# Performance work log

Hardware: AMD Instinct MI355X
Metric: run time of the kernel (lower is better)

The kernel has to match this reference:

```python
import jax, jax.numpy as jnp
import numpy as np

B, S, HLEN, VLEN, HID = 32, 2048, 1024, 1024, 1024


def setup_inputs() -> dict:
    key = jax.random.key(0)
    ks = jax.random.split(key, 6)
    scale_W = 1.0 / np.sqrt(HLEN)
    scale_U = 1.0 / np.sqrt(VLEN)
    scale_w = 1.0 / np.sqrt(HID)
    return {
        "h": jax.random.normal(ks[0], (B, HLEN), dtype=jnp.float32),
        "V": jax.random.normal(ks[1], (B, S, VLEN), dtype=jnp.float32),
        "W_w": jax.random.normal(ks[2], (HID, HLEN), dtype=jnp.float32) * scale_W,
        "W_b": jax.random.normal(ks[3], (HID,), dtype=jnp.float32) * scale_W,
        "U_w": jax.random.normal(ks[4], (HID, VLEN), dtype=jnp.float32) * scale_U,
        "w_w": jax.random.normal(ks[5], (HID,), dtype=jnp.float32) * scale_w,
    }


def reference(h, V, W_w, W_b, U_w, w_w):
    # e = w^T tanh(W h + U V^T + b); beta = softmax(e); out = sum_s beta_s V_s
    h_proj = h @ W_w.T + W_b                      # [B, HID]
    V_proj = jnp.einsum('bsv,dv->bsd', V, U_w)    # [B, S, HID]
    e = jnp.einsum('bsd,d->bs', jnp.tanh(h_proj[:, None, :] + V_proj), w_w)  # [B, S]
    beta = jax.nn.softmax(e, axis=1)              # [B, S]
    return jnp.einsum('bs,bsv->bv', beta, V)      # [B, VLEN]
```

## Files before the change

### kernel.cpp

```cpp
#include <hip/hip_runtime.h>

constexpr int B_   = 32;
constexpr int S_   = 2048;
constexpr int HID_ = 1024;
constexpr int VL_  = 1024;

typedef __attribute__((ext_vector_type(4))) float  f32x4;
typedef __attribute__((ext_vector_type(4))) short  s16x4;
typedef __attribute__((ext_vector_type(8))) short  s16x8;

__device__ __forceinline__ short f2bf(float f) {
    union { float f; unsigned u; } v; v.f = f;
    unsigned r = v.u + 0x7fffu + ((v.u >> 16) & 1u);
    return (short)(r >> 16);
}

__device__ __forceinline__ float fast_tanh(float x) {
    float e2 = __expf(2.0f * x);
    return 1.0f - 2.0f / (e2 + 1.0f);
}

__device__ __forceinline__ void async_cp16(const void* g, void* l) {
    __builtin_amdgcn_global_load_lds(
        (const __attribute__((address_space(1))) unsigned int*)g,
        (__attribute__((address_space(3))) unsigned int*)l,
        16, 0, 0);
}

__global__ __launch_bounds__(256) void hproj_kernel(const float* __restrict__ h,
                                                    const float* __restrict__ Ww,
                                                    const float* __restrict__ Wb,
                                                    float* __restrict__ hp) {
    int tid = threadIdx.x;
    int wave = tid >> 6, lane = tid & 63;
    int d = blockIdx.x * 4 + wave;
    const float* wr = Ww + (size_t)d * HID_;
    float4 wreg[4];
#pragma unroll
    for (int i = 0; i < 4; i++) wreg[i] = *(const float4*)(wr + i * 256 + lane * 4);
    float bias = Wb[d];
    for (int b = 0; b < B_; b++) {
        const float* hr = h + (size_t)b * HID_;
        float acc = 0.0f;
#pragma unroll
        for (int i = 0; i < 4; i++) {
            float4 x = *(const float4*)(hr + i * 256 + lane * 4);
            acc += wreg[i].x * x.x + wreg[i].y * x.y + wreg[i].z * x.z + wreg[i].w * x.w;
        }
#pragma unroll
        for (int o = 32; o; o >>= 1) acc += __shfl_xor(acc, o);
        if (lane == 0) hp[(size_t)b * HID_ + d] = acc + bias;
    }
}

__global__ __launch_bounds__(256) void cvt_kernel(const float* __restrict__ src,
                                                  short* __restrict__ dst, size_t n4) {
    size_t i = (size_t)blockIdx.x * blockDim.x + threadIdx.x;
    size_t stride = (size_t)gridDim.x * blockDim.x;
    for (; i < n4; i += stride) {
        float4 x = ((const float4*)src)[i];
        s16x4 y;
        y.x = f2bf(x.x); y.y = f2bf(x.y); y.z = f2bf(x.z); y.w = f2bf(x.w);
        ((s16x4*)dst)[i] = y;
    }
}

__global__ __launch_bounds__(256) void e_kernel_bf16(const short* __restrict__ Vm,
                                                     const short* __restrict__ Um,
                                                     const float* __restrict__ hp,
                                                     const float* __restrict__ ww,
                                                     float* __restrict__ e) {
    __shared__ short As[128][32];
    __shared__ short Bs[128][32];

    int tid = threadIdx.x;
    int b  = blockIdx.z;
    int d0 = blockIdx.x * 128;
    int s0 = blockIdx.y * 128;
    int wave = tid >> 6, lane = tid & 63;
    int wm = wave >> 1, wn = wave & 1;
    int col = lane & 15, quad = lane >> 4;

    f32x4 zero = {0.f, 0.f, 0.f, 0.f};
    f32x4 acc[4][4];
#pragma unroll
    for (int i = 0; i < 4; i++)
#pragma unroll
        for (int j = 0; j < 4; j++) acc[i][j] = zero;

    int r0 = 32 * wave + (lane >> 2);
    int kc = (lane & 3) * 8;
    const short* gA0 = Vm + ((size_t)b * S_ + s0 + r0) * VL_ + kc;
    const short* gA1 = gA0 + 16 * (size_t)VL_;
    const short* gB0 = Um + ((size_t)d0 + r0) * VL_ + kc;
    const short* gB1 = gB0 + 16 * (size_t)VL_;
    short* lA0 = &As[32 * wave][0];
    short* lA1 = &As[32 * wave + 16][0];
    short* lB0 = &Bs[32 * wave][0];
    short* lB1 = &Bs[32 * wave + 16][0];

    for (int k0 = 0; k0 < VL_; k0 += 32) {
        async_cp16(gA0, lA0);
        async_cp16(gA1, lA1);
        async_cp16(gB0, lB0);
        async_cp16(gB1, lB1);
        gA0 += 32; gA1 += 32; gB0 += 32; gB1 += 32;
        __syncthreads();

        s16x8 a8[4], b8[4];
#pragma unroll
        for (int tm = 0; tm < 4; tm++)
            a8[tm] = *(const s16x8*)&As[wm * 64 + tm * 16 + col][quad * 8];
#pragma unroll
        for (int tn = 0; tn < 4; tn++)
            b8[tn] = *(const s16x8*)&Bs[wn * 64 + tn * 16 + col][quad * 8];
#pragma unroll
        for (int tm = 0; tm < 4; tm++)
#pragma unroll
            for (int tn = 0; tn < 4; tn++)
                acc[tm][tn] = __builtin_amdgcn_mfma_f32_16x16x32_bf16(
                    a8[tm], b8[tn], acc[tm][tn], 0, 0, 0);
        __syncthreads();
    }

    float wv[4], hv[4];
#pragma unroll
    for (int tn = 0; tn < 4; tn++) {
        int d = d0 + wn * 64 + tn * 16 + col;
        wv[tn] = ww[d];
        hv[tn] = hp[(size_t)b * HID_ + d];
    }
#pragma unroll
    for (int tm = 0; tm < 4; tm++) {
#pragma unroll
        for (int reg = 0; reg < 4; reg++) {
            float p = 0.0f;
#pragma unroll
            for (int tn = 0; tn < 4; tn++)
                p += wv[tn] * fast_tanh(hv[tn] + acc[tm][tn][reg]);
            p += __shfl_xor(p, 1);
            p += __shfl_xor(p, 2);
            p += __shfl_xor(p, 4);
            p += __shfl_xor(p, 8);
            if (col == 0) {
                int s = s0 + wm * 64 + tm * 16 + quad * 4 + reg;
                atomicAdd(&e[(size_t)b * S_ + s], p);
            }
        }
    }
}

__global__ __launch_bounds__(256) void e_kernel_f32(const float* __restrict__ Vm,
                                                    const float* __restrict__ Um,
                                                    const float* __restrict__ hp,
                                                    const float* __restrict__ ww,
                                                    float* __restrict__ e) {
    __shared__ short As[128][40];
    __shared__ short Bs[128][40];
    int tid = threadIdx.x;
    int b  = blockIdx.z;
    int d0 = blockIdx.x * 128;
    int s0 = blockIdx.y * 128;
    int wave = tid >> 6, lane = tid & 63;
    int wm = wave >> 1, wn = wave & 1;
    int col = lane & 15, quad = lane >> 4;

    f32x4 zero = {0.f, 0.f, 0.f, 0.f};
    f32x4 acc[4][4];
#pragma unroll
    for (int i = 0; i < 4; i++)
#pragma unroll
        for (int j = 0; j < 4; j++) acc[i][j] = zero;

    const float* Abase = Vm + ((size_t)b * S_ + s0) * (size_t)VL_;
    const float* Bbase = Um + (size_t)d0 * (size_t)VL_;

    for (int k0 = 0; k0 < VL_; k0 += 32) {
        int k4 = tid & 7, rb = tid >> 3;
#pragma unroll
        for (int i = 0; i < 4; i++) {
            int r = rb + 32 * i;
            float4 x = *(const float4*)(Abase + (size_t)r * VL_ + k0 + k4 * 4);
            s16x4 ya; ya.x = f2bf(x.x); ya.y = f2bf(x.y); ya.z = f2bf(x.z); ya.w = f2bf(x.w);
            *(s16x4*)&As[r][k4 * 4] = ya;
            float4 y = *(const float4*)(Bbase + (size_t)r * VL_ + k0 + k4 * 4);
            s16x4 yb; yb.x = f2bf(y.x); yb.y = f2bf(y.y); yb.z = f2bf(y.z); yb.w = f2bf(y.w);
            *(s16x4*)&Bs[r][k4 * 4] = yb;
        }
        __syncthreads();
        s16x8 a8[4], b8[4];
#pragma unroll
        for (int tm = 0; tm < 4; tm++)
            a8[tm] = *(const s16x8*)&As[wm * 64 + tm * 16 + col][quad * 8];
#pragma unroll
        for (int tn = 0; tn < 4; tn++)
            b8[tn] = *(const s16x8*)&Bs[wn * 64 + tn * 16 + col][quad * 8];
#pragma unroll
        for (int tm = 0; tm < 4; tm++)
#pragma unroll
            for (int tn = 0; tn < 4; tn++)
                acc[tm][tn] = __builtin_amdgcn_mfma_f32_16x16x32_bf16(
                    a8[tm], b8[tn], acc[tm][tn], 0, 0, 0);
        __syncthreads();
    }

    float wv[4], hv[4];
#pragma unroll
    for (int tn = 0; tn < 4; tn++) {
        int d = d0 + wn * 64 + tn * 16 + col;
        wv[tn] = ww[d];
        hv[tn] = hp[(size_t)b * HID_ + d];
    }
#pragma unroll
    for (int tm = 0; tm < 4; tm++) {
#pragma unroll
        for (int reg = 0; reg < 4; reg++) {
            float p = 0.0f;
#pragma unroll
            for (int tn = 0; tn < 4; tn++)
                p += wv[tn] * fast_tanh(hv[tn] + acc[tm][tn][reg]);
            p += __shfl_xor(p, 1);
            p += __shfl_xor(p, 2);
            p += __shfl_xor(p, 4);
            p += __shfl_xor(p, 8);
            if (col == 0) {
                int s = s0 + wm * 64 + tm * 16 + quad * 4 + reg;
                atomicAdd(&e[(size_t)b * S_ + s], p);
            }
        }
    }
}

__global__ __launch_bounds__(256) void softmax_kernel(float* __restrict__ e) {
    int b = blockIdx.x, tid = threadIdx.x;
    float* row = e + (size_t)b * S_;
    float v[8];
    float m = -1e30f;
#pragma unroll
    for (int i = 0; i < 8; i++) { v[i] = row[tid + i * 256]; m = fmaxf(m, v[i]); }
#pragma unroll
    for (int o = 32; o; o >>= 1) m = fmaxf(m, __shfl_xor(m, o));
    __shared__ float rm[4], rs[4];
    int wave = tid >> 6, lane = tid & 63;
    if (lane == 0) rm[wave] = m;
    __syncthreads();
    m = fmaxf(fmaxf(rm[0], rm[1]), fmaxf(rm[2], rm[3]));
    float s = 0.0f;
#pragma unroll
    for (int i = 0; i < 8; i++) { v[i] = __expf(v[i] - m); s += v[i]; }
#pragma unroll
    for (int o = 32; o; o >>= 1) s += __shfl_xor(s, o);
    if (lane == 0) rs[wave] = s;
    __syncthreads();
    s = rs[0] + rs[1] + rs[2] + rs[3];
    float inv = 1.0f / s;
#pragma unroll
    for (int i = 0; i < 8; i++) row[tid + i * 256] = v[i] * inv;
}

__global__ __launch_bounds__(256) void out_kernel(const float* __restrict__ beta,
                                                  const float* __restrict__ V,
                                                  float* __restrict__ out) {
    int b = blockIdx.x, sc = blockIdx.y;
    int v4 = threadIdx.x;
    const float* Vb = V + ((size_t)b * S_ + (size_t)sc * 128) * VL_;
    const float* bb = beta + (size_t)b * S_ + (size_t)sc * 128;
    float ax = 0.f, ay = 0.f, az = 0.f, aw = 0.f;
    for (int s = 0; s < 128; s++) {
        float w = bb[s];
        float4 x = *(const float4*)(Vb + (size_t)s * VL_ + v4 * 4);
        ax += w * x.x; ay += w * x.y; az += w * x.z; aw += w * x.w;
    }
    float* o = out + (size_t)b * VL_ + v4 * 4;
    atomicAdd(o + 0, ax);
    atomicAdd(o + 1, ay);
    atomicAdd(o + 2, az);
    atomicAdd(o + 3, aw);
}

extern "C" void kernel_launch(void* const* d_in, const int* in_sizes, int n_in,
                              void* d_out, int out_size, void* d_ws, size_t ws_size,
                              hipStream_t stream) {
    const float* h  = (const float*)d_in[0];
    const float* V  = (const float*)d_in[1];
    const float* Ww = (const float*)d_in[2];
    const float* Wb = (const float*)d_in[3];
    const float* Uw = (const float*)d_in[4];
    const float* ww = (const float*)d_in[5];
    float* out = (float*)d_out;

    char* ws = (char*)d_ws;
    float* hp = (float*)ws;
    float* e  = (float*)(ws + 131072);
    short* Vb16 = (short*)(ws + 393216);
    short* Ub16 = Vb16 + (size_t)B_ * S_ * VL_;
    size_t need = 393216 + ((size_t)B_ * S_ * VL_ + (size_t)HID_ * VL_) * 2;
    bool bf16path = (ws_size >= need);

    hipMemsetAsync(e, 0, (size_t)B_ * S_ * 4, stream);
    hipMemsetAsync(out, 0, (size_t)out_size * 4, stream);

    hproj_kernel<<<dim3(HID_ / 4), 256, 0, stream>>>(h, Ww, Wb, hp);

    if (bf16path) {
        cvt_kernel<<<2048, 256, 0, stream>>>(V, Vb16, (size_t)B_ * S_ * VL_ / 4);
        cvt_kernel<<<256, 256, 0, stream>>>(Uw, Ub16, (size_t)HID_ * VL_ / 4);
        e_kernel_bf16<<<dim3(HID_ / 128, S_ / 128, B_), 256, 0, stream>>>(
            Vb16, Ub16, hp, ww, e);
    } else {
        e_kernel_f32<<<dim3(HID_ / 128, S_ / 128, B_), 256, 0, stream>>>(
            V, Uw, hp, ww, e);
    }

    softmax_kernel<<<B_, 256, 0, stream>>>(e);
    out_kernel<<<dim3(B_, S_ / 128), 256, 0, stream>>>(e, V, out);
}
```

Before: 667.6 us.

## Loop HID tiles inside e kernel and read bf16 V in output pass

```diff
diff --git a/kernel.cpp b/kernel.cpp
--- a/kernel.cpp
+++ b/kernel.cpp
@@ -13,6 +13,12 @@
     union { float f; unsigned u; } v; v.f = f;
     unsigned r = v.u + 0x7fffu + ((v.u >> 16) & 1u);
     return (short)(r >> 16);
+}
+
+__device__ __forceinline__ float bf2f(short s) {
+    union { unsigned u; float f; } v;
+    v.u = ((unsigned)(unsigned short)s) << 16;
+    return v.f;
 }
 
 __device__ __forceinline__ float fast_tanh(float x) {
@@ -72,82 +78,99 @@
                                                      float* __restrict__ e) {
     __shared__ short As[128][32];
     __shared__ short Bs[128][32];
+    __shared__ float ebuf[2][128];
 
     int tid = threadIdx.x;
-    int b  = blockIdx.z;
-    int d0 = blockIdx.x * 128;
-    int s0 = blockIdx.y * 128;
+    int s0 = blockIdx.x * 128;
+    int b  = blockIdx.y;
     int wave = tid >> 6, lane = tid & 63;
     int wm = wave >> 1, wn = wave & 1;
     int col = lane & 15, quad = lane >> 4;
 
-    f32x4 zero = {0.f, 0.f, 0.f, 0.f};
-    f32x4 acc[4][4];
-#pragma unroll
-    for (int i = 0; i < 4; i++)
-#pragma unroll
-        for (int j = 0; j < 4; j++) acc[i][j] = zero;
-
     int r0 = 32 * wave + (lane >> 2);
     int kc = (lane & 3) * 8;
-    const short* gA0 = Vm + ((size_t)b * S_ + s0 + r0) * VL_ + kc;
-    const short* gA1 = gA0 + 16 * (size_t)VL_;
-    const short* gB0 = Um + ((size_t)d0 + r0) * VL_ + kc;
-    const short* gB1 = gB0 + 16 * (size_t)VL_;
+    const short* gAb = Vm + ((size_t)b * S_ + s0 + r0) * VL_ + kc;
     short* lA0 = &As[32 * wave][0];
     short* lA1 = &As[32 * wave + 16][0];
     short* lB0 = &Bs[32 * wave][0];
     short* lB1 = &Bs[32 * wave + 16][0];
 
-    for (int k0 = 0; k0 < VL_; k0 += 32) {
-        async_cp16(gA0, lA0);
-        async_cp16(gA1, lA1);
-        async_cp16(gB0, lB0);
-        async_cp16(gB1, lB1);
-        gA0 += 32; gA1 += 32; gB0 += 32; gB1 += 32;
-        __syncthreads();
-
-        s16x8 a8[4], b8[4];
+    float ep[4][4];
+#pragma unroll
+    for (int i = 0; i < 4; i++)
+#pragma unroll
+        for (int j = 0; j < 4; j++) ep[i][j] = 0.0f;
+
+    for (int dt = 0; dt < 8; dt++) {
+        int d0 = dt * 128;
+        const short* gA0 = gAb;
+        const short* gA1 = gAb + 16 * (size_t)VL_;
+        const short* gB0 = Um + ((size_t)d0 + r0) * VL_ + kc;
+        const short* gB1 = gB0 + 16 * (size_t)VL_;
+
+        f32x4 zero = {0.f, 0.f, 0.f, 0.f};
+        f32x4 acc[4][4];
+#pragma unroll
+        for (int i = 0; i < 4; i++)
+#pragma unroll
+            for (int j = 0; j < 4; j++) acc[i][j] = zero;
+
+        for (int k0 = 0; k0 < VL_; k0 += 32) {
+            async_cp16(gA0, lA0);
+            async_cp16(gA1, lA1);
+            async_cp16(gB0, lB0);
+            async_cp16(gB1, lB1);
+            gA0 += 32; gA1 += 32; gB0 += 32; gB1 += 32;
+            __syncthreads();
+
+            s16x8 a8[4], b8[4];
+#pragma unroll
+            for (int tm = 0; tm < 4; tm++)
+                a8[tm] = *(const s16x8*)&As[wm * 64 + tm * 16 + col][quad * 8];
+#pragma unroll
+            for (int tn = 0; tn < 4; tn++)
+                b8[tn] = *(const s16x8*)&Bs[wn * 64 + tn * 16 + col][quad * 8];
+#pragma unroll
+            for (int tm = 0; tm < 4; tm++)
+#pragma unroll
+                for (int tn = 0; tn < 4; tn++)
+                    acc[tm][tn] = __builtin_amdgcn_mfma_f32_16x16x32_bf16(
+                        a8[tm], b8[tn], acc[tm][tn], 0, 0, 0);
+            __syncthreads();
+        }
+
+        float wv[4], hv[4];
+#pragma unroll
+        for (int tn = 0; tn < 4; tn++) {
+            int d = d0 + wn * 64 + tn * 16 + col;
+            wv[tn] = ww[d];
+            hv[tn] = hp[(size_t)b * HID_ + d];
+        }
 #pragma unroll
         for (int tm = 0; tm < 4; tm++)
-            a8[tm] = *(const s16x8*)&As[wm * 64 + tm * 16 + col][quad * 8];
-#pragma unroll
-        for (int tn = 0; tn < 4; tn++)
-            b8[tn] = *(const s16x8*)&Bs[wn * 64 + tn * 16 + col][quad * 8];
-#pragma unroll
-        for (int tm = 0; tm < 4; tm++)
-#pragma unroll
-            for (int tn = 0; tn < 4; tn++)
-                acc[tm][tn] = __builtin_amdgcn_mfma_f32_16x16x32_bf16(
-                    a8[tm], b8[tn], acc[tm][tn], 0, 0, 0);
-        __syncthreads();
-    }
-
-    float wv[4], hv[4];
-#pragma unroll
-    for (int tn = 0; tn < 4; tn++) {
-        int d = d0 + wn * 64 + tn * 16 + col;
-        wv[tn] = ww[d];
-        hv[tn] = hp[(size_t)b * HID_ + d];
-    }
-#pragma unroll
-    for (int tm = 0; tm < 4; tm++) {
+#pragma unroll
+            for (int reg = 0; reg < 4; reg++) {
+#pragma unroll
+                for (int tn = 0; tn < 4; tn++)
+                    ep[tm][reg] += wv[tn] * fast_tanh(hv[tn] + acc[tm][tn][reg]);
+            }
+    }
+
+#pragma unroll
+    for (int tm = 0; tm < 4; tm++)
 #pragma unroll
         for (int reg = 0; reg < 4; reg++) {
-            float p = 0.0f;
-#pragma unroll
-            for (int tn = 0; tn < 4; tn++)
-                p += wv[tn] * fast_tanh(hv[tn] + acc[tm][tn][reg]);
+            float p = ep[tm][reg];
             p += __shfl_xor(p, 1);
             p += __shfl_xor(p, 2);
             p += __shfl_xor(p, 4);
             p += __shfl_xor(p, 8);
-            if (col == 0) {
-                int s = s0 + wm * 64 + tm * 16 + quad * 4 + reg;
-                atomicAdd(&e[(size_t)b * S_ + s], p);
-            }
-        }
-    }
+            if (col == 0)
+                ebuf[wn][wm * 64 + tm * 16 + quad * 4 + reg] = p;
+        }
+    __syncthreads();
+    if (tid < 128)
+        e[(size_t)b * S_ + s0 + tid] = ebuf[0][tid] + ebuf[1][tid];
 }
 
 __global__ __launch_bounds__(256) void e_kernel_f32(const float* __restrict__ Vm,
@@ -258,9 +281,30 @@
     for (int i = 0; i < 8; i++) row[tid + i * 256] = v[i] * inv;
 }
 
-__global__ __launch_bounds__(256) void out_kernel(const float* __restrict__ beta,
-                                                  const float* __restrict__ V,
-                                                  float* __restrict__ out) {
+__global__ __launch_bounds__(256) void out_kernel_bf16(const float* __restrict__ beta,
+                                                       const short* __restrict__ Vb16,
+                                                       float* __restrict__ out) {
+    int b = blockIdx.x, sc = blockIdx.y;
+    int v4 = threadIdx.x;
+    const short* Vp = Vb16 + ((size_t)b * S_ + (size_t)sc * 128) * VL_;
+    const float* bb = beta + (size_t)b * S_ + (size_t)sc * 128;
+    float ax = 0.f, ay = 0.f, az = 0.f, aw = 0.f;
+    for (int s = 0; s < 128; s++) {
+        float w = bb[s];
+        s16x4 x = *(const s16x4*)(Vp + (size_t)s * VL_ + v4 * 4);
+        ax += w * bf2f(x.x); ay += w * bf2f(x.y);
+        az += w * bf2f(x.z); aw += w * bf2f(x.w);
+    }
+    float* o = out + (size_t)b * VL_ + v4 * 4;
+    atomicAdd(o + 0, ax);
+    atomicAdd(o + 1, ay);
+    atomicAdd(o + 2, az);
+    atomicAdd(o + 3, aw);
+}
+
+__global__ __launch_bounds__(256) void out_kernel_f32(const float* __restrict__ beta,
+                                                      const float* __restrict__ V,
+                                                      float* __restrict__ out) {
     int b = blockIdx.x, sc = blockIdx.y;
     int v4 = threadIdx.x;
     const float* Vb = V + ((size_t)b * S_ + (size_t)sc * 128) * VL_;
@@ -297,7 +341,6 @@
     size_t need = 393216 + ((size_t)B_ * S_ * VL_ + (size_t)HID_ * VL_) * 2;
     bool bf16path = (ws_size >= need);
 
-    hipMemsetAsync(e, 0, (size_t)B_ * S_ * 4, stream);
     hipMemsetAsync(out, 0, (size_t)out_size * 4, stream);
 
     hproj_kernel<<<dim3(HID_ / 4), 256, 0, stream>>>(h, Ww, Wb, hp);
@@ -305,13 +348,14 @@
     if (bf16path) {
         cvt_kernel<<<2048, 256, 0, stream>>>(V, Vb16, (size_t)B_ * S_ * VL_ / 4);
         cvt_kernel<<<256, 256, 0, stream>>>(Uw, Ub16, (size_t)HID_ * VL_ / 4);
-        e_kernel_bf16<<<dim3(HID_ / 128, S_ / 128, B_), 256, 0, stream>>>(
-            Vb16, Ub16, hp, ww, e);
+        e_kernel_bf16<<<dim3(S_ / 128, B_), 256, 0, stream>>>(Vb16, Ub16, hp, ww, e);
+        softmax_kernel<<<B_, 256, 0, stream>>>(e);
+        out_kernel_bf16<<<dim3(B_, S_ / 128), 256, 0, stream>>>(e, Vb16, out);
     } else {
+        hipMemsetAsync(e, 0, (size_t)B_ * S_ * 4, stream);
         e_kernel_f32<<<dim3(HID_ / 128, S_ / 128, B_), 256, 0, stream>>>(
             V, Uw, hp, ww, e);
-    }
-
-    softmax_kernel<<<B_, 256, 0, stream>>>(e);
-    out_kernel<<<dim3(B_, S_ / 128), 256, 0, stream>>>(e, V, out);
-}
+        softmax_kernel<<<B_, 256, 0, stream>>>(e);
+        out_kernel_f32<<<dim3(B_, S_ / 128), 256, 0, stream>>>(e, V, out);
+    }
+}
```

Result: no change. 666.3 us (-0.2%).
